# Kernel optimization log

Measured on AMD Instinct MI355X. Metric: run time of the kernel, lower is better.

## Reference

```python
import jax, jax.numpy as jnp
import numpy as np

KG_E = 200000
IN_DIM = 256
OUT_DIM = 128
B = 20000
N_RAND = 620000  # random edges; self-loops appended -> total 640000


def setup_inputs() -> dict:
    key = jax.random.key(0)
    ks = jax.random.split(key, 8)
    ent_embed = jax.random.normal(ks[0], (KG_E, IN_DIM), dtype=jnp.float32)
    batch_ids = jax.random.randint(ks[1], (B,), 0, KG_E, dtype=jnp.int64)
    # random edges: rows are batch-local [0,B), cols are global [0,KG_E)
    rand_rows = jax.random.randint(ks[2], (N_RAND,), 0, B, dtype=jnp.int64)
    rand_cols = jax.random.randint(ks[3], (N_RAND,), 0, KG_E, dtype=jnp.int64)
    # self-loops as in drop_neigh: row=node_num, col=batch_ids
    rows = jnp.concatenate([rand_rows, jnp.arange(B, dtype=jnp.int64)])
    cols = jnp.concatenate([rand_cols, batch_ids])
    edge_index = jnp.stack([rows, cols])  # [2, E]
    W = jax.random.normal(ks[4], (OUT_DIM, IN_DIM), dtype=jnp.float32) * (1.0 / np.sqrt(IN_DIM))
    b = jax.random.normal(ks[5], (OUT_DIM,), dtype=jnp.float32) * 0.01
    w_atten_r = jax.random.normal(ks[6], (2 * OUT_DIM, 1), dtype=jnp.float32) * 0.1
    prelu_w = jnp.full((1,), 0.25, dtype=jnp.float32)
    return {"ent_embed": ent_embed, "batch_ids": batch_ids, "edge_index": edge_index,
            "W": W, "b": b, "w_atten_r": w_atten_r, "prelu_w": prelu_w}


def reference(ent_embed, batch_ids, edge_index, W, b, w_atten_r, prelu_w):
    # gat_in = Linear(ent_embed): [KG_E, out]
    gat_in = ent_embed @ W.T + b
    rows = edge_index[0]  # batch-local [0,B)
    cols = edge_index[1]  # global [0,KG_E)
    left = gat_in[batch_ids[rows]]   # [E, out]  (left_embed[edge_index[0]])
    right = gat_in[cols]             # [E, out]
    # concat([left,right]) @ w_atten_r  ==  left@w_a[:out] + right@w_a[out:]
    score = (left @ w_atten_r[:OUT_DIM] + right @ w_atten_r[OUT_DIM:])[:, 0]  # [E]
    att = jnp.exp(-jax.nn.leaky_relu(score, negative_slope=0.2))
    nB = batch_ids.shape[0]
    # special_spmm with ones(KG_E,1): per-row sum of attention
    e_rowsum = jax.ops.segment_sum(att, rows, num_segments=nB)  # [B]
    # special_spmm with gat_in: attention-weighted neighbor aggregation
    e_out = jax.ops.segment_sum(att[:, None] * right, rows, num_segments=nB)  # [B, out]
    e_out = e_out / e_rowsum[:, None]
    # PReLU with single learnable scalar
    return jnp.where(e_out >= 0, e_out, prelu_w[0] * e_out)
```

## Files before the change

kernel.cpp:

```cpp
#include <hip/hip_runtime.h>

#define KG_E   200000
#define IN_DIM 256
#define OUT_DIM 128
#define BATCH  20000
#define NEDGE  640000
#define BUCKET 128

typedef unsigned short ushort_t;
typedef __attribute__((ext_vector_type(8))) short bf16x8;
typedef __attribute__((ext_vector_type(4))) float f32x4;
typedef __attribute__((ext_vector_type(4))) int   i32x4;

__device__ __forceinline__ float bf2f(unsigned int u) {
  return __builtin_bit_cast(float, u << 16);
}
__device__ __forceinline__ unsigned short f2bf(float f) {
  unsigned int x = __builtin_bit_cast(unsigned int, f);
  x += 0x7FFFu + ((x >> 16) & 1u);
  return (unsigned short)(x >> 16);
}
__device__ __forceinline__ int idx_at(const void* p, long long i, int is64) {
  return is64 ? (int)((const long long*)p)[i] : ((const int*)p)[i];
}
__device__ __forceinline__ float fld(const void* p, int i, int isf32) {
  return isf32 ? ((const float*)p)[i] : bf2f(((const ushort_t*)p)[i]);
}
__device__ __forceinline__ bf16x8 pack8(f32x4 a, f32x4 b) {
  bf16x8 r;
#pragma unroll
  for (int j = 0; j < 4; j++) {
    ((ushort_t*)&r)[j]     = f2bf(a[j]);
    ((ushort_t*)&r)[4 + j] = f2bf(b[j]);
  }
  return r;
}

__global__ __launch_bounds__(64) void detect_kernel(const void* __restrict__ ent,
                                                    const void* __restrict__ edge,
                                                    int* __restrict__ flags) {
  int lane = threadIdx.x;
  const ushort_t* u = (const ushort_t*)ent;
  int plaus = 0;
#pragma unroll
  for (int i = 0; i < 4; i++) {
    int e = (u[2 * (lane * 4 + i)] >> 7) & 0xff;
    if (e >= 113 && e <= 141) plaus++;
  }
  const int* ei = (const int*)edge;
  int nz = (ei[2 * lane + 1] != 0) ? 1 : 0;
#pragma unroll
  for (int m = 32; m >= 1; m >>= 1) {
    plaus += __shfl_xor(plaus, m);
    nz    += __shfl_xor(nz, m);
  }
  if (lane == 0) {
    flags[0] = (plaus >= 128) ? 0 : 1;
    flags[1] = (nz == 0) ? 1 : 0;
  }
}

__global__ __launch_bounds__(512, 4) void gemm_kernel(
    const void* __restrict__ ent, const void* __restrict__ W,
    const void* __restrict__ bias, const void* __restrict__ w_atten,
    const int* __restrict__ flags, ushort_t* __restrict__ gat,
    float* __restrict__ sRn, float* __restrict__ sLn,
    int* __restrict__ cursor)
{
  __shared__ __align__(16) unsigned char lds[65536];
  const int isf32 = flags[0];
  const int tid  = threadIdx.x;
  const int lane = tid & 63;
  const int w    = tid >> 6;
  const int l16  = lane & 15;
  const int quad = lane >> 4;
  const int m0   = blockIdx.x * 128;

  if (blockIdx.x < (BATCH + 511) / 512) {
    int zi = blockIdx.x * 512 + tid;
    if (zi < BATCH) cursor[zi] = 0;
  }

#pragma unroll
  for (int i = 0; i < 8; i++) {
    int L = i * 512 + tid;
    int r = L >> 5, s = L & 31;
    bf16x8 v;
    if (isf32) {
      const float* bp = (const float*)W + r * 256 + s * 8;
      v = pack8(*(const f32x4*)bp, *(const f32x4*)(bp + 4));
    } else {
      v = *(const bf16x8*)((const ushort_t*)W + r * 256 + s * 8);
    }
    *(bf16x8*)(lds + r * 512 + ((s ^ (r & 15)) * 16)) = v;
  }
  __syncthreads();

  const int row0 = m0 + w * 16;
  int arow = row0 + l16; arow = arow < KG_E ? arow : (KG_E - 1);

  f32x4 acc[8];
#pragma unroll
  for (int nt = 0; nt < 8; nt++) acc[nt] = (f32x4){0.f, 0.f, 0.f, 0.f};

#define MFMA_STEP(AF, KS)                                                     \
  do {                                                                        \
    _Pragma("unroll") for (int nt = 0; nt < 8; nt++) {                        \
      bf16x8 bf = *(const bf16x8*)(lds + (nt * 16 + l16) * 512 +              \
                                   ((((KS) * 4 + quad) ^ l16) * 16));         \
      acc[nt] = __builtin_amdgcn_mfma_f32_16x16x32_bf16(AF, bf, acc[nt], 0, 0, 0); \
    }                                                                         \
  } while (0)

  if (isf32) {
    const float* ap = (const float*)ent + (size_t)arow * IN_DIM + quad * 8;
    f32x4 b0[4], b1[4];
#pragma unroll
    for (int p = 0; p < 4; p++) {
      b0[p] = *(const f32x4*)(ap + p * 32);
      b1[p] = *(const f32x4*)(ap + p * 32 + 4);
    }
#pragma unroll
    for (int ks = 0; ks < 8; ks++) {
      bf16x8 af = pack8(b0[ks & 3], b1[ks & 3]);
      if (ks < 4) {
        b0[ks & 3] = *(const f32x4*)(ap + (ks + 4) * 32);
        b1[ks & 3] = *(const f32x4*)(ap + (ks + 4) * 32 + 4);
      }
      MFMA_STEP(af, ks);
    }
  } else {
    const ushort_t* ap = (const ushort_t*)ent + (size_t)arow * IN_DIM + quad * 8;
    bf16x8 ab[4];
#pragma unroll
    for (int p = 0; p < 4; p++) ab[p] = *(const bf16x8*)(ap + p * 32);
#pragma unroll
    for (int ks = 0; ks < 8; ks++) {
      bf16x8 af = ab[ks & 3];
      if (ks < 4) ab[ks & 3] = *(const bf16x8*)(ap + (ks + 4) * 32);
      MFMA_STEP(af, ks);
    }
  }
#undef MFMA_STEP

  float bv[8], w1v[8], w2v[8];
#pragma unroll
  for (int nt = 0; nt < 8; nt++) {
    int c = nt * 16 + l16;
    bv[nt]  = fld(bias, c, isf32);
    w1v[nt] = fld(w_atten, c, isf32);
    w2v[nt] = fld(w_atten, OUT_DIM + c, isf32);
  }
  float pr[4] = {0.f, 0.f, 0.f, 0.f}, pl[4] = {0.f, 0.f, 0.f, 0.f};
#pragma unroll
  for (int nt = 0; nt < 8; nt++)
#pragma unroll
    for (int reg = 0; reg < 4; reg++) {
      float v = acc[nt][reg] + bv[nt];
      acc[nt][reg] = v;
      pr[reg] += v * w2v[nt];
      pl[reg] += v * w1v[nt];
    }
#pragma unroll
  for (int m = 1; m < 16; m <<= 1)
#pragma unroll
    for (int reg = 0; reg < 4; reg++) {
      pr[reg] += __shfl_xor(pr[reg], m);
      pl[reg] += __shfl_xor(pl[reg], m);
    }
  if (l16 == 0) {
#pragma unroll
    for (int reg = 0; reg < 4; reg++) {
      int r = row0 + quad * 4 + reg;
      if (r < KG_E) { sRn[r] = pr[reg]; sLn[r] = pl[reg]; }
    }
  }

  __syncthreads();
#pragma unroll
  for (int nt = 0; nt < 8; nt++)
#pragma unroll
    for (int reg = 0; reg < 4; reg++)
      *(ushort_t*)(lds + (w * 16 + quad * 4 + reg) * 272 + (nt * 16 + l16) * 2) =
          f2bf(acc[nt][reg]);
  __syncthreads();
#pragma unroll
  for (int i = 0; i < 4; i++) {
    int L = i * 512 + tid;
    int rl = L >> 4, cs = L & 15;
    int gr = m0 + rl;
    if (gr < KG_E) {
      f32x4 v = *(const f32x4*)(lds + rl * 272 + cs * 16);
      *(f32x4*)((char*)gat + (size_t)gr * 256 + cs * 16) = v;
    }
  }
}

__global__ __launch_bounds__(256) void scatter_kernel(
    const void* __restrict__ edge, const void* __restrict__ batch_ids,
    const int* __restrict__ flags, const float* __restrict__ sLn,
    const float* __restrict__ sRn, int* __restrict__ cursor,
    int2* __restrict__ colatt)
{
  const int is64 = flags[1];
  int e = blockIdx.x * 256 + threadIdx.x;
  if (e >= NEDGE) return;
  int r = idx_at(edge, e, is64);
  r = r < 0 ? 0 : (r >= BATCH ? BATCH - 1 : r);
  int c = idx_at(edge, (long long)NEDGE + e, is64);
  c = c < 0 ? 0 : (c >= KG_E ? KG_E - 1 : c);
  int b = idx_at(batch_ids, r, is64);
  b = b < 0 ? 0 : (b >= KG_E ? KG_E - 1 : b);
  float score = sLn[b] + sRn[c];
  float lr = score > 0.f ? score : 0.2f * score;
  lr = lr > 80.f ? 80.f : (lr < -80.f ? -80.f : lr);
  float att = __expf(-lr);
  int p = atomicAdd(&cursor[r], 1);
  if (p < BUCKET)
    colatt[(size_t)r * BUCKET + p] = make_int2(c, __builtin_bit_cast(int, att));
}

__global__ __launch_bounds__(256) void aggregate_kernel(
    const ushort_t* __restrict__ gat, const int* __restrict__ colatt,
    const int* __restrict__ cursor, const void* __restrict__ prelu,
    const int* __restrict__ flags, float* __restrict__ out)
{
  const int isf32 = flags[0];
  const int row  = __builtin_amdgcn_readfirstlane(blockIdx.x * 4 + (threadIdx.x >> 6));
  const int lane = threadIdx.x & 63;
  const int h    = lane >> 5;
  const int sub  = lane & 31;
  int cnt = __builtin_amdgcn_readfirstlane(cursor[row]);
  cnt = cnt < BUCKET ? cnt : BUCKET;
  const i32x4* ca4 = (const i32x4*)(colatt + (size_t)row * (BUCKET * 2));

  float acc0 = 0.f, acc1 = 0.f, acc2 = 0.f, acc3 = 0.f, rowsum = 0.f;

#define EDGE_PAIR(QQ)                                                         \
  do {                                                                        \
    int c_ = h ? (QQ).z : (QQ).x;                                             \
    float a_ = __builtin_bit_cast(float, h ? (QQ).w : (QQ).y);                \
    unsigned long long pk_ =                                                  \
        *(const unsigned long long*)(gat + (size_t)c_ * OUT_DIM + 4 * sub);   \
    acc0 += a_ * bf2f((unsigned int)(pk_ & 0xffffu));                         \
    acc1 += a_ * bf2f((unsigned int)((pk_ >> 16) & 0xffffu));                 \
    acc2 += a_ * bf2f((unsigned int)((pk_ >> 32) & 0xffffu));                 \
    acc3 += a_ * bf2f((unsigned int)(pk_ >> 48));                             \
    rowsum += a_;                                                             \
  } while (0)

  int j = 0;
  for (; j + 8 <= cnt; j += 8) {
    i32x4 q0 = ca4[(j >> 1) + 0];
    i32x4 q1 = ca4[(j >> 1) + 1];
    i32x4 q2 = ca4[(j >> 1) + 2];
    i32x4 q3 = ca4[(j >> 1) + 3];
    EDGE_PAIR(q0); EDGE_PAIR(q1); EDGE_PAIR(q2); EDGE_PAIR(q3);
  }
  for (; j < cnt; j += 2) {
    i32x4 q = ca4[j >> 1];
    int c_ = h ? q.z : q.x;
    c_ = c_ < 0 ? 0 : (c_ >= KG_E ? KG_E - 1 : c_);
    float a_ = ((j + h) < cnt) ? __builtin_bit_cast(float, h ? q.w : q.y) : 0.f;
    unsigned long long pk_ =
        *(const unsigned long long*)(gat + (size_t)c_ * OUT_DIM + 4 * sub);
    acc0 += a_ * bf2f((unsigned int)(pk_ & 0xffffu));
    acc1 += a_ * bf2f((unsigned int)((pk_ >> 16) & 0xffffu));
    acc2 += a_ * bf2f((unsigned int)((pk_ >> 32) & 0xffffu));
    acc3 += a_ * bf2f((unsigned int)(pk_ >> 48));
    rowsum += a_;
  }
#undef EDGE_PAIR

  acc0 += __shfl_xor(acc0, 32);
  acc1 += __shfl_xor(acc1, 32);
  acc2 += __shfl_xor(acc2, 32);
  acc3 += __shfl_xor(acc3, 32);
  rowsum += __shfl_xor(rowsum, 32);

  if (h == 0) {
    float inv = rowsum > 0.f ? 1.0f / rowsum : 0.f;
    float pw = fld(prelu, 0, isf32);
    f32x4 v;
    float t0 = acc0 * inv, t1 = acc1 * inv, t2 = acc2 * inv, t3 = acc3 * inv;
    v[0] = t0 >= 0.f ? t0 : pw * t0;
    v[1] = t1 >= 0.f ? t1 : pw * t1;
    v[2] = t2 >= 0.f ? t2 : pw * t2;
    v[3] = t3 >= 0.f ? t3 : pw * t3;
    *(f32x4*)(out + (size_t)row * OUT_DIM + 4 * sub) = v;
  }
}

extern "C" void kernel_launch(void* const* d_in, const int* in_sizes, int n_in,
                              void* d_out, int out_size, void* d_ws, size_t ws_size,
                              hipStream_t stream) {
  const void* ent       = d_in[0];
  const void* batch_ids = d_in[1];
  const void* edge      = d_in[2];
  const void* W         = d_in[3];
  const void* bias      = d_in[4];
  const void* w_atten   = d_in[5];
  const void* prelu     = d_in[6];
  float*      out       = (float*)d_out;

  char* p = (char*)d_ws;
  int* flags     = (int*)p;       p += 64;
  ushort_t* gat  = (ushort_t*)p;  p += (size_t)KG_E * OUT_DIM * 2;
  float* sRn     = (float*)p;     p += (size_t)KG_E * 4;
  float* sLn     = (float*)p;     p += (size_t)KG_E * 4;
  int* cursor    = (int*)p;       p += (size_t)BATCH * 4;
  p = (char*)(((size_t)p + 15) & ~(size_t)15);
  int2* colatt   = (int2*)p;      p += (size_t)BATCH * BUCKET * 8;

  detect_kernel<<<dim3(1), dim3(64), 0, stream>>>(ent, edge, flags);
  gemm_kernel<<<dim3((KG_E + 127) / 128), dim3(512), 0, stream>>>(
      ent, W, bias, w_atten, flags, gat, sRn, sLn, cursor);
  scatter_kernel<<<dim3(NEDGE / 256), dim3(256), 0, stream>>>(
      edge, batch_ids, flags, sLn, sRn, cursor, colatt);
  aggregate_kernel<<<dim3(BATCH / 4), dim3(256), 0, stream>>>(
      gat, (const int*)colatt, cursor, prelu, flags, out);
}
```

Baseline: 381.2 us.

## Inline dtype detection, widen aggregate gathers, and process two edges per scatter thread

Removes the separate detect kernel launch and flags buffer, so each kernel detects the float and index dtypes itself with wave ballots. The aggregate kernel now gathers 16-byte bf16x8 chunks, with four edges handled per wave step instead of two, and reduces across quads with shuffles. The scatter kernel handles two edges per thread with half as many blocks. The changes aim to cut launch overhead and make gathers wider, at the cost of repeated detection work in every wave and more accumulator registers.

Result: no change. 384.5 us (+0.9%).

```diff
diff --git a/kernel.cpp b/kernel.cpp
--- a/kernel.cpp
+++ b/kernel.cpp
@@ -36,39 +36,31 @@
   return r;
 }
 
-__global__ __launch_bounds__(64) void detect_kernel(const void* __restrict__ ent,
-                                                    const void* __restrict__ edge,
-                                                    int* __restrict__ flags) {
-  int lane = threadIdx.x;
+__device__ __forceinline__ int detect_f32_wave(const void* ent) {
+  int lane = threadIdx.x & 63;
   const ushort_t* u = (const ushort_t*)ent;
-  int plaus = 0;
+  int cnt = 0;
 #pragma unroll
   for (int i = 0; i < 4; i++) {
     int e = (u[2 * (lane * 4 + i)] >> 7) & 0xff;
-    if (e >= 113 && e <= 141) plaus++;
-  }
-  const int* ei = (const int*)edge;
-  int nz = (ei[2 * lane + 1] != 0) ? 1 : 0;
-#pragma unroll
-  for (int m = 32; m >= 1; m >>= 1) {
-    plaus += __shfl_xor(plaus, m);
-    nz    += __shfl_xor(nz, m);
-  }
-  if (lane == 0) {
-    flags[0] = (plaus >= 128) ? 0 : 1;
-    flags[1] = (nz == 0) ? 1 : 0;
-  }
+    cnt += __popcll(__ballot(e >= 113 && e <= 141));
+  }
+  return (cnt >= 128) ? 0 : 1;
+}
+__device__ __forceinline__ int detect_i64_wave(const void* edge) {
+  int lane = threadIdx.x & 63;
+  int nz = ((const int*)edge)[2 * lane + 1] != 0;
+  return (__ballot(nz) == 0ULL) ? 1 : 0;
 }
 
 __global__ __launch_bounds__(512, 4) void gemm_kernel(
     const void* __restrict__ ent, const void* __restrict__ W,
     const void* __restrict__ bias, const void* __restrict__ w_atten,
-    const int* __restrict__ flags, ushort_t* __restrict__ gat,
-    float* __restrict__ sRn, float* __restrict__ sLn,
+    ushort_t* __restrict__ gat, float* __restrict__ sRn, float* __restrict__ sLn,
     int* __restrict__ cursor)
 {
   __shared__ __align__(16) unsigned char lds[65536];
-  const int isf32 = flags[0];
+  const int isf32 = detect_f32_wave(ent);
   const int tid  = threadIdx.x;
   const int lane = tid & 63;
   const int w    = tid >> 6;
@@ -198,96 +190,91 @@
 
 __global__ __launch_bounds__(256) void scatter_kernel(
     const void* __restrict__ edge, const void* __restrict__ batch_ids,
-    const int* __restrict__ flags, const float* __restrict__ sLn,
-    const float* __restrict__ sRn, int* __restrict__ cursor,
-    int2* __restrict__ colatt)
+    const float* __restrict__ sLn, const float* __restrict__ sRn,
+    int* __restrict__ cursor, int2* __restrict__ colatt)
 {
-  const int is64 = flags[1];
-  int e = blockIdx.x * 256 + threadIdx.x;
+  const int is64 = detect_i64_wave(edge);
+  long long e = (long long)(blockIdx.x * 256 + threadIdx.x) * 2;
   if (e >= NEDGE) return;
-  int r = idx_at(edge, e, is64);
-  r = r < 0 ? 0 : (r >= BATCH ? BATCH - 1 : r);
-  int c = idx_at(edge, (long long)NEDGE + e, is64);
-  c = c < 0 ? 0 : (c >= KG_E ? KG_E - 1 : c);
-  int b = idx_at(batch_ids, r, is64);
-  b = b < 0 ? 0 : (b >= KG_E ? KG_E - 1 : b);
-  float score = sLn[b] + sRn[c];
-  float lr = score > 0.f ? score : 0.2f * score;
-  lr = lr > 80.f ? 80.f : (lr < -80.f ? -80.f : lr);
-  float att = __expf(-lr);
-  int p = atomicAdd(&cursor[r], 1);
-  if (p < BUCKET)
-    colatt[(size_t)r * BUCKET + p] = make_int2(c, __builtin_bit_cast(int, att));
+#pragma unroll
+  for (int t = 0; t < 2; t++) {
+    int r = idx_at(edge, e + t, is64);
+    r = r < 0 ? 0 : (r >= BATCH ? BATCH - 1 : r);
+    int c = idx_at(edge, (long long)NEDGE + e + t, is64);
+    c = c < 0 ? 0 : (c >= KG_E ? KG_E - 1 : c);
+    int b = idx_at(batch_ids, r, is64);
+    b = b < 0 ? 0 : (b >= KG_E ? KG_E - 1 : b);
+    float score = sLn[b] + sRn[c];
+    float lr = score > 0.f ? score : 0.2f * score;
+    lr = lr > 80.f ? 80.f : (lr < -80.f ? -80.f : lr);
+    float att = __expf(-lr);
+    int p = atomicAdd(&cursor[r], 1);
+    if (p < BUCKET)
+      colatt[(size_t)r * BUCKET + p] = make_int2(c, __builtin_bit_cast(int, att));
+  }
 }
 
 __global__ __launch_bounds__(256) void aggregate_kernel(
     const ushort_t* __restrict__ gat, const int* __restrict__ colatt,
     const int* __restrict__ cursor, const void* __restrict__ prelu,
-    const int* __restrict__ flags, float* __restrict__ out)
+    const void* __restrict__ ent, float* __restrict__ out)
 {
-  const int isf32 = flags[0];
+  const int isf32 = detect_f32_wave(ent);
   const int row  = __builtin_amdgcn_readfirstlane(blockIdx.x * 4 + (threadIdx.x >> 6));
   const int lane = threadIdx.x & 63;
-  const int h    = lane >> 5;
-  const int sub  = lane & 31;
+  const int quad = lane >> 4;
+  const int l16  = lane & 15;
   int cnt = __builtin_amdgcn_readfirstlane(cursor[row]);
   cnt = cnt < BUCKET ? cnt : BUCKET;
   const i32x4* ca4 = (const i32x4*)(colatt + (size_t)row * (BUCKET * 2));
 
-  float acc0 = 0.f, acc1 = 0.f, acc2 = 0.f, acc3 = 0.f, rowsum = 0.f;
-
-#define EDGE_PAIR(QQ)                                                         \
-  do {                                                                        \
-    int c_ = h ? (QQ).z : (QQ).x;                                             \
-    float a_ = __builtin_bit_cast(float, h ? (QQ).w : (QQ).y);                \
-    unsigned long long pk_ =                                                  \
-        *(const unsigned long long*)(gat + (size_t)c_ * OUT_DIM + 4 * sub);   \
-    acc0 += a_ * bf2f((unsigned int)(pk_ & 0xffffu));                         \
-    acc1 += a_ * bf2f((unsigned int)((pk_ >> 16) & 0xffffu));                 \
-    acc2 += a_ * bf2f((unsigned int)((pk_ >> 32) & 0xffffu));                 \
-    acc3 += a_ * bf2f((unsigned int)(pk_ >> 48));                             \
-    rowsum += a_;                                                             \
+  float acc[8] = {0.f, 0.f, 0.f, 0.f, 0.f, 0.f, 0.f, 0.f};
+  float rowsum = 0.f;
+
+#define DO4(J, GUARD)                                                          \
+  do {                                                                         \
+    i32x4 q_ = ca4[((J) >> 1) + (quad >> 1)];                                  \
+    int   c_ = (quad & 1) ? q_.z : q_.x;                                       \
+    float a_ = __builtin_bit_cast(float, (quad & 1) ? q_.w : q_.y);            \
+    if (GUARD) {                                                               \
+      if ((J) + quad >= cnt) a_ = 0.f;                                         \
+      c_ = c_ < 0 ? 0 : (c_ >= KG_E ? KG_E - 1 : c_);                          \
+    }                                                                          \
+    bf16x8 g_ = *(const bf16x8*)(gat + (size_t)c_ * OUT_DIM + l16 * 8);        \
+    _Pragma("unroll") for (int k = 0; k < 8; k++)                              \
+        acc[k] += a_ * bf2f(((const ushort_t*)&g_)[k]);                        \
+    rowsum += a_;                                                              \
   } while (0)
 
   int j = 0;
-  for (; j + 8 <= cnt; j += 8) {
-    i32x4 q0 = ca4[(j >> 1) + 0];
-    i32x4 q1 = ca4[(j >> 1) + 1];
-    i32x4 q2 = ca4[(j >> 1) + 2];
-    i32x4 q3 = ca4[(j >> 1) + 3];
-    EDGE_PAIR(q0); EDGE_PAIR(q1); EDGE_PAIR(q2); EDGE_PAIR(q3);
-  }
-  for (; j < cnt; j += 2) {
-    i32x4 q = ca4[j >> 1];
-    int c_ = h ? q.z : q.x;
-    c_ = c_ < 0 ? 0 : (c_ >= KG_E ? KG_E - 1 : c_);
-    float a_ = ((j + h) < cnt) ? __builtin_bit_cast(float, h ? q.w : q.y) : 0.f;
-    unsigned long long pk_ =
-        *(const unsigned long long*)(gat + (size_t)c_ * OUT_DIM + 4 * sub);
-    acc0 += a_ * bf2f((unsigned int)(pk_ & 0xffffu));
-    acc1 += a_ * bf2f((unsigned int)((pk_ >> 16) & 0xffffu));
-    acc2 += a_ * bf2f((unsigned int)((pk_ >> 32) & 0xffffu));
-    acc3 += a_ * bf2f((unsigned int)(pk_ >> 48));
-    rowsum += a_;
-  }
-#undef EDGE_PAIR
-
-  acc0 += __shfl_xor(acc0, 32);
-  acc1 += __shfl_xor(acc1, 32);
-  acc2 += __shfl_xor(acc2, 32);
-  acc3 += __shfl_xor(acc3, 32);
-  rowsum += __shfl_xor(rowsum, 32);
-
-  if (h == 0) {
+  for (; j + 8 <= cnt; j += 8) { DO4(j, 0); DO4(j + 4, 0); }
+  for (; j < cnt; j += 4) DO4(j, 1);
+#undef DO4
+
+#pragma unroll
+  for (int m = 16; m <= 32; m <<= 1) {
+#pragma unroll
+    for (int k = 0; k < 8; k++) acc[k] += __shfl_xor(acc[k], m);
+    rowsum += __shfl_xor(rowsum, m);
+  }
+
+  if (quad == 0) {
     float inv = rowsum > 0.f ? 1.0f / rowsum : 0.f;
     float pw = fld(prelu, 0, isf32);
-    f32x4 v;
-    float t0 = acc0 * inv, t1 = acc1 * inv, t2 = acc2 * inv, t3 = acc3 * inv;
-    v[0] = t0 >= 0.f ? t0 : pw * t0;
-    v[1] = t1 >= 0.f ? t1 : pw * t1;
-    v[2] = t2 >= 0.f ? t2 : pw * t2;
-    v[3] = t3 >= 0.f ? t3 : pw * t3;
-    *(f32x4*)(out + (size_t)row * OUT_DIM + 4 * sub) = v;
+    f32x4 v0, v1;
+#pragma unroll
+    for (int k = 0; k < 4; k++) {
+      float t = acc[k] * inv;
+      v0[k] = t >= 0.f ? t : pw * t;
+    }
+#pragma unroll
+    for (int k = 0; k < 4; k++) {
+      float t = acc[4 + k] * inv;
+      v1[k] = t >= 0.f ? t : pw * t;
+    }
+    float* op = out + (size_t)row * OUT_DIM + l16 * 8;
+    *(f32x4*)op = v0;
+    *(f32x4*)(op + 4) = v1;
   }
 }
 
@@ -304,7 +291,6 @@
   float*      out       = (float*)d_out;
 
   char* p = (char*)d_ws;
-  int* flags     = (int*)p;       p += 64;
   ushort_t* gat  = (ushort_t*)p;  p += (size_t)KG_E * OUT_DIM * 2;
   float* sRn     = (float*)p;     p += (size_t)KG_E * 4;
   float* sLn     = (float*)p;     p += (size_t)KG_E * 4;
@@ -312,11 +298,10 @@
   p = (char*)(((size_t)p + 15) & ~(size_t)15);
   int2* colatt   = (int2*)p;      p += (size_t)BATCH * BUCKET * 8;
 
-  detect_kernel<<<dim3(1), dim3(64), 0, stream>>>(ent, edge, flags);
   gemm_kernel<<<dim3((KG_E + 127) / 128), dim3(512), 0, stream>>>(
-      ent, W, bias, w_atten, flags, gat, sRn, sLn, cursor);
-  scatter_kernel<<<dim3(NEDGE / 256), dim3(256), 0, stream>>>(
-      edge, batch_ids, flags, sLn, sRn, cursor, colatt);
+      ent, W, bias, w_atten, gat, sRn, sLn, cursor);
+  scatter_kernel<<<dim3(NEDGE / 512), dim3(256), 0, stream>>>(
+      edge, batch_ids, sLn, sRn, cursor, colatt);
   aggregate_kernel<<<dim3(BATCH / 4), dim3(256), 0, stream>>>(
-      gat, (const int*)colatt, cursor, prelu, flags, out);
-}
+      gat, (const int*)colatt, cursor, prelu, ent, out);
+}
```
